# Kernel optimization log

Hardware: AMD Instinct MI355X
Metric: run time of the kernel (lower is better)

Reference implementation:

```python
import jax, jax.numpy as jnp
import numpy as np

N = 20000   # nodes
E = 320000  # edges (before self-loops)
D = 256     # feature width (inChl = hdChl = outChl)
H = 4       # heads
C = D // H  # per-head channels = 64
NEG_SLOPE = 0.2
LN_EPS = 1e-5


def setup_inputs() -> dict:
    key = jax.random.key(0)
    ks = jax.random.split(key, 2 + 4 * 4)
    inp = {}
    inp["x"] = jax.random.normal(ks[0], (1, N, D), dtype=jnp.float32)
    inp["edge_index"] = jax.random.randint(ks[1], (2, E), 0, N, dtype=jnp.int32)
    s = 1.0 / np.sqrt(D)
    for i in range(4):
        k = 2 + 4 * i
        inp[f"Wl{i+1}"] = (jax.random.normal(ks[k], (D, H * C), dtype=jnp.float32) * s)
        inp[f"Wr{i+1}"] = (jax.random.normal(ks[k + 1], (D, H * C), dtype=jnp.float32) * s)
        inp[f"att{i+1}"] = (jax.random.normal(ks[k + 2], (H, C), dtype=jnp.float32) * s)
        inp[f"b{i+1}"] = jnp.zeros((H * C,), dtype=jnp.float32)
        inp[f"g{i+1}"] = jnp.ones((D,), dtype=jnp.float32)
        inp[f"be{i+1}"] = jnp.zeros((D,), dtype=jnp.float32)
    return inp


def _segment_softmax(scores, seg, num_segments):
    # scores: [E, H], per-destination softmax over incoming edges
    m = jax.ops.segment_max(scores, seg, num_segments=num_segments)
    e = jnp.exp(scores - m[seg])
    d = jax.ops.segment_sum(e, seg, num_segments=num_segments)
    return e / d[seg]


def _gatv2(x, src, dst, Wl, Wr, att, b):
    # GATv2Conv defaults: share_weights=False, concat=True, negative_slope=0.2
    n = x.shape[0]
    xl = (x @ Wl).reshape(n, H, C)  # source transform
    xr = (x @ Wr).reshape(n, H, C)  # target transform
    m = xl[src] + xr[dst]                                  # [E', H, C]
    e = jnp.sum(jax.nn.leaky_relu(m, NEG_SLOPE) * att, -1) # [E', H]
    alpha = _segment_softmax(e, dst, n)                    # [E', H]
    out = jax.ops.segment_sum(xl[src] * alpha[:, :, None], dst, num_segments=n)
    return out.reshape(n, H * C) + b


def _layernorm(x, g, b):
    mu = jnp.mean(x, -1, keepdims=True)
    var = jnp.mean(jnp.square(x - mu), -1, keepdims=True)
    return (x - mu) * jax.lax.rsqrt(var + LN_EPS) * g + b


def _forward(x, edge_index, layers):
    h = x[0]  # squeeze batch dim -> [N, D]
    n = h.shape[0]
    loop = jnp.arange(n, dtype=edge_index.dtype)
    src = jnp.concatenate([edge_index[0], loop])  # add_self_loops=True
    dst = jnp.concatenate([edge_index[1], loop])
    for (Wl, Wr, att, b, g, be) in layers:
        h = _gatv2(h, src, dst, Wl, Wr, att, b)
        h = jax.nn.relu(_layernorm(h, g, be))
    return h[None]  # unsqueeze -> [1, N, D]


def reference(x, edge_index,
              Wl1, Wr1, att1, b1, g1, be1,
              Wl2, Wr2, att2, b2, g2, be2,
              Wl3, Wr3, att3, b3, g3, be3,
              Wl4, Wr4, att4, b4, g4, be4):
    layers = [(Wl1, Wr1, att1, b1, g1, be1),
              (Wl2, Wr2, att2, b2, g2, be2),
              (Wl3, Wr3, att3, b3, g3, be3),
              (Wl4, Wr4, att4, b4, g4, be4)]
    return _forward(x, edge_index, layers)
```

## Files before the change

kernel.cpp:

```cpp
#include <hip/hip_runtime.h>
#include <math.h>

#define N_NODES 20000
#define E_EDGES 320000
#define EP (E_EDGES + N_NODES)
#define D 256
#define NHEAD 4
#define CH 64
#define NEG_SLOPE 0.2f
#define LN_EPS 1e-5f

typedef _Float16 half8_t __attribute__((ext_vector_type(8)));
typedef _Float16 half4_t __attribute__((ext_vector_type(4)));
typedef _Float16 half2_t __attribute__((ext_vector_type(2)));
typedef float   float4_t __attribute__((ext_vector_type(4)));
typedef int     iv4_t    __attribute__((ext_vector_type(4)));

#define SCATTER_BLOCKS ((EP + 255) / 256)

__device__ __forceinline__ void async_cp16(const void* g, void* l)
{
    __builtin_amdgcn_global_load_lds(
        (const __attribute__((address_space(1))) void*)g,
        (__attribute__((address_space(3))) void*)l, 16, 0, 0);
}

template<int CTRL>
__device__ __forceinline__ float dpp_add(float v) {
    int t = __builtin_amdgcn_update_dpp(0, __float_as_int(v), CTRL, 0xF, 0xF, true);
    return v + __int_as_float(t);
}
__device__ __forceinline__ float grp8_sum(float v) {
    v = dpp_add<0xB1>(v);
    v = dpp_add<0x4E>(v);
    v = dpp_add<0x141>(v);
    return v;
}

__device__ __forceinline__ iv4_t load_idx4(const int* p) {
    iv4_t v;
    __builtin_memcpy(&v, p, 16);
    return v;
}

__device__ __forceinline__ float dot_att8(half8_t t, const half2_t a0, const half2_t a1,
                                          const half2_t a2, const half2_t a3) {
    half2_t t01 = {t[0], t[1]}, t23 = {t[2], t[3]};
    half2_t t45 = {t[4], t[5]}, t67 = {t[6], t[7]};
    float v = __builtin_amdgcn_fdot2(t01, a0, 0.0f, false);
    v = __builtin_amdgcn_fdot2(t23, a1, v, false);
    v = __builtin_amdgcn_fdot2(t45, a2, v, false);
    return __builtin_amdgcn_fdot2(t67, a3, v, false);
}

__global__ __launch_bounds__(256)
void convert_hist_kernel(const float* __restrict__ x, _Float16* __restrict__ h16,
                         const int* __restrict__ ei, int* __restrict__ deg)
{
    int i = blockIdx.x * 256 + threadIdx.x;
    if (i < EP) {
        int dst = (i < E_EDGES) ? ei[E_EDGES + i] : (i - E_EDGES);
        atomicAdd(&deg[dst], 1);
    }
    if (i >= N_NODES * D / 4) return;
    float4 v = reinterpret_cast<const float4*>(x)[i];
    half4_t o;
    o.x = (_Float16)v.x; o.y = (_Float16)v.y; o.z = (_Float16)v.z; o.w = (_Float16)v.w;
    reinterpret_cast<half4_t*>(h16)[i] = o;
}

__global__ __launch_bounds__(1024)
void csr_scan_kernel(const int* __restrict__ deg, int* __restrict__ rowptr,
                     int* __restrict__ cursor, int* __restrict__ csr_src)
{
    __shared__ int buf[5120];
    __shared__ int wsum[16];
    __shared__ int carry_s;
    int t = threadIdx.x, lane = t & 63, w = t >> 6;
    if (t == 0) carry_s = 0;
    if (t < 8) csr_src[EP + t] = 0;

    for (int c = 0; c < 4; ++c) {
        int base = c * 5120;
        #pragma unroll
        for (int k = 0; k < 5; ++k) {
            int idx = base + k * 1024 + t;
            buf[k * 1024 + t] = (idx < N_NODES) ? deg[idx] : 0;
        }
        __syncthreads();
        int loc[5]; int s = 0;
        #pragma unroll
        for (int k = 0; k < 5; ++k) { loc[k] = buf[t * 5 + k]; s += loc[k]; }
        int x = s;
        #pragma unroll
        for (int o = 1; o < 64; o <<= 1) {
            int y = __shfl_up(x, o, 64);
            if (lane >= o) x += y;
        }
        if (lane == 63) wsum[w] = x;
        __syncthreads();
        if (t == 0) {
            int sa = carry_s;
            #pragma unroll
            for (int k = 0; k < 16; ++k) { int tmp = wsum[k]; wsum[k] = sa; sa += tmp; }
            carry_s = sa;
        }
        __syncthreads();
        int excl = wsum[w] + x - s;
        #pragma unroll
        for (int k = 0; k < 5; ++k) { buf[t * 5 + k] = excl; excl += loc[k]; }
        __syncthreads();
        #pragma unroll
        for (int k = 0; k < 5; ++k) {
            int idx = base + k * 1024 + t;
            if (idx < N_NODES) {
                int v = buf[k * 1024 + t];
                rowptr[idx] = v;
                cursor[idx] = v;
            }
        }
        __syncthreads();
    }
    if (t == 0) rowptr[N_NODES] = carry_s;
}

struct WPtrs { const float* p[8]; };
__global__ __launch_bounds__(256)
void scatter_convw_kernel(const int* __restrict__ ei, int* __restrict__ cursor,
                          int* __restrict__ csr_src, WPtrs wp,
                          _Float16* __restrict__ Wt_all)
{
    if (blockIdx.x < SCATTER_BLOCKS) {
        int e = blockIdx.x * 256 + threadIdx.x;
        if (e >= EP) return;
        int src, dst;
        if (e < E_EDGES) { src = ei[e]; dst = ei[E_EDGES + e]; }
        else             { src = dst = e - E_EDGES; }
        int pos = atomicAdd(&cursor[dst], 1);
        csr_src[pos] = src;
        return;
    }
    __shared__ float tile[64][65];
    int bz = blockIdx.x - SCATTER_BLOCKS;
    int bxi = bz & 3, byi = (bz >> 2) & 3, z = bz >> 4;
    const float* W = wp.p[z];
    _Float16* out = Wt_all + (size_t)z * 65536;
    int bx = bxi * 64, by = byi * 64;
    int t = threadIdx.x;
    #pragma unroll
    for (int i = 0; i < 16; ++i) {
        int idx = t + i * 256;
        int kk = idx >> 6, nn = idx & 63;
        tile[kk][nn] = W[(by + kk) * 256 + bx + nn];
    }
    __syncthreads();
    #pragma unroll
    for (int i = 0; i < 16; ++i) {
        int idx = t + i * 256;
        int nn = idx >> 6, kk = idx & 63;
        out[(bx + nn) * 256 + by + kk] = (_Float16)tile[kk][nn];
    }
}

#define BM 128
#define BN 128
#define BK 64
#define EPAD2 72
__global__ __launch_bounds__(256)
void gemm_f16_kernel(const _Float16* __restrict__ A16, const _Float16* __restrict__ Wt,
                     _Float16* __restrict__ X0, _Float16* __restrict__ X1, int nrows)
{
    const int b = blockIdx.x;
    const int pair = ((b >> 4) << 3) + (b & 7);
    const int z = (b >> 3) & 1;
    if (pair >= 314) return;
    const int yb = (pair >= 157) ? 1 : 0;
    const int xb = pair - yb * 157;

    const _Float16* W = Wt + z * 65536 + yb * (BN * 256);
    _Float16* X = z ? X1 : X0;
    const int row0 = xb * BM;
    const int col0 = yb * BN;

    __shared__ __align__(1024) char smem[BM * BK * 2 + BN * BK * 2];
    _Float16 (*As)[BK] = reinterpret_cast<_Float16 (*)[BK]>(smem);
    _Float16 (*Bs)[BK] = reinterpret_cast<_Float16 (*)[BK]>(smem + BM * BK * 2);
    _Float16* As_flat = reinterpret_cast<_Float16*>(smem);
    _Float16* Bs_flat = reinterpret_cast<_Float16*>(smem + BM * BK * 2);
    _Float16* ep = reinterpret_cast<_Float16*>(smem);

    const int tid  = threadIdx.x;
    const int wave = tid >> 6, lane = tid & 63;
    const int wy = wave >> 1, wx = wave & 1;
    const int quad = lane >> 4, l16 = lane & 15;

    float4_t acc[4][4];
    #pragma unroll
    for (int i = 0; i < 4; ++i)
        #pragma unroll
        for (int j = 0; j < 4; ++j) acc[i][j] = (float4_t)0.0f;

    const int r_in  = lane >> 3;
    const int c_in  = (lane & 7) * 8;

    #pragma unroll
    for (int k0 = 0; k0 < 256; k0 += BK) {
        #pragma unroll
        for (int j = 0; j < 4; ++j) {
            int ia  = wave * 4 + j;
            int row = ia * 8 + r_in;
            int gra = row0 + row;
            gra = (gra < nrows) ? gra : (nrows - 1);
            async_cp16(A16 + (size_t)gra * 256 + k0 + c_in, As_flat + ia * 512);
            async_cp16(W   + (size_t)row * 256 + k0 + c_in, Bs_flat + ia * 512);
        }
        __syncthreads();

        #pragma unroll
        for (int s = 0; s < 2; ++s) {
            half8_t af[4], bf[4];
            #pragma unroll
            for (int i = 0; i < 4; ++i)
                af[i] = *reinterpret_cast<const half8_t*>(&As[wy * 64 + i * 16 + l16][s * 32 + quad * 8]);
            #pragma unroll
            for (int j = 0; j < 4; ++j)
                bf[j] = *reinterpret_cast<const half8_t*>(&Bs[wx * 64 + j * 16 + l16][s * 32 + quad * 8]);
            #pragma unroll
            for (int i = 0; i < 4; ++i)
                #pragma unroll
                for (int j = 0; j < 4; ++j)
                    acc[i][j] = __builtin_amdgcn_mfma_f32_16x16x32_f16(af[i], bf[j], acc[i][j], 0, 0, 0);
        }
        __syncthreads();
    }

    _Float16* epw = ep + wave * 16 * EPAD2;
    #pragma unroll
    for (int it = 0; it < 4; ++it) {
        #pragma unroll
        for (int j = 0; j < 4; ++j)
            #pragma unroll
            for (int r = 0; r < 4; ++r)
                epw[(quad * 4 + r) * EPAD2 + j * 16 + l16] = (_Float16)acc[it][j][r];
        #pragma unroll
        for (int p = 0; p < 2; ++p) {
            int row = p * 8 + (lane >> 3);
            int col = (lane & 7) * 8;
            int gr = row0 + wy * 64 + it * 16 + row;
            half8_t v = *reinterpret_cast<const half8_t*>(&epw[row * EPAD2 + col]);
            if (gr < nrows)
                *reinterpret_cast<half8_t*>(X + gr * 256 + col0 + wx * 64 + col) = v;
        }
    }
}

__global__ __launch_bounds__(256)
void gat_fused_kernel(const _Float16* __restrict__ xl, const _Float16* __restrict__ xr,
                      const int* __restrict__ rowptr, const int* __restrict__ csr_src,
                      const float* __restrict__ att,
                      const float* __restrict__ bias, const float* __restrict__ g,
                      const float* __restrict__ be,
                      float* __restrict__ out32, _Float16* __restrict__ out16,
                      int write32)
{
    const int tid = threadIdx.x;
    const int w = tid >> 6, lane = tid & 63;
    const int n = blockIdx.x * 4 + w;
    const int hs  = lane >> 5;
    const int l32 = lane & 31;
    const int c0  = l32 * 8;
    const int start = rowptr[n], end = rowptr[n + 1];

    half8_t xrv = *reinterpret_cast<const half8_t*>(xr + (size_t)n * D + c0);
    half2_t at0, at1, at2, at3;
    {
        float4 a0 = *reinterpret_cast<const float4*>(att + c0);
        float4 a1 = *reinterpret_cast<const float4*>(att + c0 + 4);
        at0 = half2_t{(_Float16)a0.x, (_Float16)a0.y};
        at1 = half2_t{(_Float16)a0.z, (_Float16)a0.w};
        at2 = half2_t{(_Float16)a1.x, (_Float16)a1.y};
        at3 = half2_t{(_Float16)a1.z, (_Float16)a1.w};
    }
    const _Float16 slope = (_Float16)NEG_SLOPE;

    float den = 0.0f;
    float num[8];
    #pragma unroll
    for (int k = 0; k < 8; ++k) num[k] = 0.0f;

    int i = start;
    iv4_t nxt = load_idx4(csr_src + i + 4 * hs);
    for (; i + 8 <= end; i += 8) {
        iv4_t cur = nxt;
        half8_t h[4];
        #pragma unroll
        for (int j = 0; j < 4; ++j)
            h[j] = *reinterpret_cast<const half8_t*>(xl + (size_t)cur[j] * D + c0);
        nxt = load_idx4(csr_src + i + 8 + 4 * hs);
        float p[4];
        #pragma unroll
        for (int j = 0; j < 4; ++j) {
            half8_t t = h[j] + xrv;
            t = __builtin_elementwise_max(t, t * slope);
            p[j] = dot_att8(t, at0, at1, at2, at3);
        }
        #pragma unroll
        for (int j = 0; j < 4; ++j) p[j] = grp8_sum(p[j]);
        #pragma unroll
        for (int j = 0; j < 4; ++j) p[j] = __expf(p[j]);
        #pragma unroll
        for (int j = 0; j < 4; ++j) {
            den += p[j];
            #pragma unroll
            for (int k = 0; k < 8; ++k)
                num[k] = fmaf(p[j], (float)h[j][k], num[k]);
        }
    }
    if (i < end) {
        iv4_t cur = nxt;
        half8_t h[4];
        #pragma unroll
        for (int j = 0; j < 4; ++j)
            h[j] = *reinterpret_cast<const half8_t*>(xl + (size_t)cur[j] * D + c0);
        float p[4];
        #pragma unroll
        for (int j = 0; j < 4; ++j) {
            half8_t t = h[j] + xrv;
            t = __builtin_elementwise_max(t, t * slope);
            p[j] = dot_att8(t, at0, at1, at2, at3);
        }
        #pragma unroll
        for (int j = 0; j < 4; ++j) p[j] = grp8_sum(p[j]);
        #pragma unroll
        for (int j = 0; j < 4; ++j) {
            float pj = (i + 4 * hs + j < end) ? __expf(p[j]) : 0.0f;
            den += pj;
            #pragma unroll
            for (int k = 0; k < 8; ++k)
                num[k] = fmaf(pj, (float)h[j][k], num[k]);
        }
    }

    den += __shfl_xor(den, 32, 64);
    #pragma unroll
    for (int k = 0; k < 8; ++k) num[k] += __shfl_xor(num[k], 32, 64);

    float inv_den = 1.0f / den;
    float4 b0 = *reinterpret_cast<const float4*>(bias + c0);
    float4 b1 = *reinterpret_cast<const float4*>(bias + c0 + 4);
    float a[8];
    a[0] = fmaf(num[0], inv_den, b0.x);
    a[1] = fmaf(num[1], inv_den, b0.y);
    a[2] = fmaf(num[2], inv_den, b0.z);
    a[3] = fmaf(num[3], inv_den, b0.w);
    a[4] = fmaf(num[4], inv_den, b1.x);
    a[5] = fmaf(num[5], inv_den, b1.y);
    a[6] = fmaf(num[6], inv_den, b1.z);
    a[7] = fmaf(num[7], inv_den, b1.w);

    float wsum = 0.0f, wsq = 0.0f;
    #pragma unroll
    for (int k = 0; k < 8; ++k) { wsum += a[k]; wsq += a[k] * a[k]; }
    #pragma unroll
    for (int o = 1; o < 32; o <<= 1) {
        wsum += __shfl_xor(wsum, o, 64);
        wsq  += __shfl_xor(wsq,  o, 64);
    }
    float mu = wsum * (1.0f / 256.0f);
    float var = wsq * (1.0f / 256.0f) - mu * mu;
    float rstd = rsqrtf(var + LN_EPS);

    float4 g0 = *reinterpret_cast<const float4*>(g + c0);
    float4 g1 = *reinterpret_cast<const float4*>(g + c0 + 4);
    float4 e0 = *reinterpret_cast<const float4*>(be + c0);
    float4 e1 = *reinterpret_cast<const float4*>(be + c0 + 4);
    float o8[8];
    o8[0] = fmaxf((a[0] - mu) * rstd * g0.x + e0.x, 0.0f);
    o8[1] = fmaxf((a[1] - mu) * rstd * g0.y + e0.y, 0.0f);
    o8[2] = fmaxf((a[2] - mu) * rstd * g0.z + e0.z, 0.0f);
    o8[3] = fmaxf((a[3] - mu) * rstd * g0.w + e0.w, 0.0f);
    o8[4] = fmaxf((a[4] - mu) * rstd * g1.x + e1.x, 0.0f);
    o8[5] = fmaxf((a[5] - mu) * rstd * g1.y + e1.y, 0.0f);
    o8[6] = fmaxf((a[6] - mu) * rstd * g1.z + e1.z, 0.0f);
    o8[7] = fmaxf((a[7] - mu) * rstd * g1.w + e1.w, 0.0f);

    float s0 = hs ? o8[4] : o8[0];
    float s1 = hs ? o8[5] : o8[1];
    float s2 = hs ? o8[6] : o8[2];
    float s3 = hs ? o8[7] : o8[3];
    if (write32) {
        float4 ov = make_float4(s0, s1, s2, s3);
        *reinterpret_cast<float4*>(out32 + (size_t)n * D + c0 + 4 * hs) = ov;
    } else {
        half4_t ov;
        ov.x = (_Float16)s0; ov.y = (_Float16)s1; ov.z = (_Float16)s2; ov.w = (_Float16)s3;
        *reinterpret_cast<half4_t*>(out16 + (size_t)n * D + c0 + 4 * hs) = ov;
    }
}

extern "C" void kernel_launch(void* const* d_in, const int* in_sizes, int n_in,
                              void* d_out, int out_size, void* d_ws, size_t ws_size,
                              hipStream_t stream)
{
    const float* x  = (const float*)d_in[0];
    const int*   ei = (const int*)d_in[1];

    char* ws = (char*)d_ws;
    size_t off = 0;
    _Float16* h16   = (_Float16*)(ws + off); off += (size_t)N_NODES * D * 2;
    _Float16* xl    = (_Float16*)(ws + off); off += (size_t)N_NODES * D * 2;
    _Float16* xr    = (_Float16*)(ws + off); off += (size_t)N_NODES * D * 2;
    _Float16* WtA   = (_Float16*)(ws + off); off += (size_t)8 * 65536 * 2;
    int* rowptr     = (int*)(ws + off);      off += (size_t)(N_NODES + 32) * 4;
    int* cursor     = (int*)(ws + off);      off += (size_t)N_NODES * 4;
    int* csr_src    = (int*)(ws + off);      off += (size_t)(EP + 32) * 4;

    WPtrs wp;
    for (int l = 0; l < 4; ++l) {
        wp.p[2 * l + 0] = (const float*)d_in[2 + 6 * l + 0];
        wp.p[2 * l + 1] = (const float*)d_in[2 + 6 * l + 1];
    }

    hipMemsetAsync(cursor, 0, (size_t)N_NODES * 4, stream);
    convert_hist_kernel<<<(N_NODES * D / 4 + 255) / 256, 256, 0, stream>>>(x, h16, ei, cursor);
    csr_scan_kernel<<<1, 1024, 0, stream>>>(cursor, rowptr, cursor, csr_src);
    scatter_convw_kernel<<<SCATTER_BLOCKS + 128, 256, 0, stream>>>(ei, cursor, csr_src, wp, WtA);

    for (int l = 0; l < 4; ++l) {
        const float* att  = (const float*)d_in[2 + 6 * l + 2];
        const float* bias = (const float*)d_in[2 + 6 * l + 3];
        const float* g    = (const float*)d_in[2 + 6 * l + 4];
        const float* be   = (const float*)d_in[2 + 6 * l + 5];

        gemm_f16_kernel<<<640, 256, 0, stream>>>(h16, WtA + (size_t)l * 131072,
                                                 xl, xr, N_NODES);
        gat_fused_kernel<<<N_NODES / 4, 256, 0, stream>>>(xl, xr, rowptr, csr_src, att,
                                                          bias, g, be,
                                                          (float*)d_out, h16, (l == 3) ? 1 : 0);
    }
}
```

Baseline: 327.9 us.

## Double-buffer GEMM LDS tiles and XOR-swizzle columns to avoid bank conflicts

The f16 MFMA GEMM now keeps two LDS buffers and issues the async global-to-LDS loads for the next K slice while the current slice is being multiplied. It also XOR-swizzles the 16-byte column chunk by row, on both the load and the read side, to reduce LDS bank conflicts on the fragment reads. This doubles LDS use to 64 KB per block, which may lower occupancy. The K loop has only four iterations, so there is little room to hide load latency.

```diff
diff --git a/kernel.cpp b/kernel.cpp
--- a/kernel.cpp
+++ b/kernel.cpp
@@ -162,10 +162,6 @@
     }
 }
 
-#define BM 128
-#define BN 128
-#define BK 64
-#define EPAD2 72
 __global__ __launch_bounds__(256)
 void gemm_f16_kernel(const _Float16* __restrict__ A16, const _Float16* __restrict__ Wt,
                      _Float16* __restrict__ X0, _Float16* __restrict__ X1, int nrows)
@@ -177,17 +173,13 @@
     const int yb = (pair >= 157) ? 1 : 0;
     const int xb = pair - yb * 157;
 
-    const _Float16* W = Wt + z * 65536 + yb * (BN * 256);
+    const _Float16* W = Wt + z * 65536 + yb * (128 * 256);
     _Float16* X = z ? X1 : X0;
-    const int row0 = xb * BM;
-    const int col0 = yb * BN;
-
-    __shared__ __align__(1024) char smem[BM * BK * 2 + BN * BK * 2];
-    _Float16 (*As)[BK] = reinterpret_cast<_Float16 (*)[BK]>(smem);
-    _Float16 (*Bs)[BK] = reinterpret_cast<_Float16 (*)[BK]>(smem + BM * BK * 2);
-    _Float16* As_flat = reinterpret_cast<_Float16*>(smem);
-    _Float16* Bs_flat = reinterpret_cast<_Float16*>(smem + BM * BK * 2);
-    _Float16* ep = reinterpret_cast<_Float16*>(smem);
+    const int row0 = xb * 128;
+    const int col0 = yb * 128;
+
+    __shared__ __align__(1024) _Float16 smem[2 * 16384];
+    _Float16* ep = smem;
 
     const int tid  = threadIdx.x;
     const int wave = tid >> 6, lane = tid & 63;
@@ -201,30 +193,39 @@
         for (int j = 0; j < 4; ++j) acc[i][j] = (float4_t)0.0f;
 
     const int r_in  = lane >> 3;
-    const int c_in  = (lane & 7) * 8;
-
-    #pragma unroll
-    for (int k0 = 0; k0 < 256; k0 += BK) {
+    const int c_sw  = (((lane & 7) ^ r_in) * 8);
+
+    auto stage = [&](int buf, int k0) {
+        _Float16* Af = smem + buf * 16384;
+        _Float16* Bf = Af + 8192;
         #pragma unroll
         for (int j = 0; j < 4; ++j) {
             int ia  = wave * 4 + j;
             int row = ia * 8 + r_in;
             int gra = row0 + row;
             gra = (gra < nrows) ? gra : (nrows - 1);
-            async_cp16(A16 + (size_t)gra * 256 + k0 + c_in, As_flat + ia * 512);
-            async_cp16(W   + (size_t)row * 256 + k0 + c_in, Bs_flat + ia * 512);
-        }
-        __syncthreads();
-
+            async_cp16(A16 + (size_t)gra * 256 + k0 + c_sw, Af + ia * 512);
+            async_cp16(W   + (size_t)row * 256 + k0 + c_sw, Bf + ia * 512);
+        }
+    };
+
+    stage(0, 0);
+    __syncthreads();
+    #pragma unroll
+    for (int kk = 0; kk < 4; ++kk) {
+        if (kk < 3) stage((kk + 1) & 1, (kk + 1) * 64);
+        const _Float16* Af = smem + (kk & 1) * 16384;
+        const _Float16* Bf = Af + 8192;
         #pragma unroll
         for (int s = 0; s < 2; ++s) {
+            const int csw_rd = (((quad + 4 * s) ^ (l16 & 7)) * 8);
             half8_t af[4], bf[4];
             #pragma unroll
             for (int i = 0; i < 4; ++i)
-                af[i] = *reinterpret_cast<const half8_t*>(&As[wy * 64 + i * 16 + l16][s * 32 + quad * 8]);
+                af[i] = *reinterpret_cast<const half8_t*>(Af + (wy * 64 + i * 16 + l16) * 64 + csw_rd);
             #pragma unroll
             for (int j = 0; j < 4; ++j)
-                bf[j] = *reinterpret_cast<const half8_t*>(&Bs[wx * 64 + j * 16 + l16][s * 32 + quad * 8]);
+                bf[j] = *reinterpret_cast<const half8_t*>(Bf + (wx * 64 + j * 16 + l16) * 64 + csw_rd);
             #pragma unroll
             for (int i = 0; i < 4; ++i)
                 #pragma unroll
@@ -234,6 +235,7 @@
         __syncthreads();
     }
 
+#define EPAD2 72
     _Float16* epw = ep + wave * 16 * EPAD2;
     #pragma unroll
     for (int it = 0; it < 4; ++it) {
```

Result: slower. 335.5 us (+2.3%).
